# Kernel optimization log

Hardware: AMD Instinct MI355X
Metric: run time of the kernel (lower is better)

The kernel has to match this reference:

```python
import jax, jax.numpy as jnp
import numpy as np

P_ASEM = 0.8
IN_SIZE = 128


def setup_inputs() -> dict:
    key = jax.random.key(0)
    k1, k2, k3, k4 = jax.random.split(key, 4)
    B, N, D = 8, 2048, IN_SIZE
    x = jax.random.normal(k1, (B, N, D), dtype=jnp.float32)
    adj = jax.random.uniform(k2, (B, N, N), dtype=jnp.float32)
    # Linear(2D -> 1): weight [1, 2D], bias [1] (torch convention). Store as vector/scalar.
    bound = 1.0 / np.sqrt(2 * D)
    W = jax.random.uniform(k3, (2 * D,), minval=-bound, maxval=bound, dtype=jnp.float32)
    b = jax.random.uniform(k4, (), minval=-bound, maxval=bound, dtype=jnp.float32)
    return {"x": x, "adj": adj, "W": W, "b": b}


def reference(x, adj, W, b):
    # linear(cat(xi, xj)) == x @ W[:D] (row term) + x @ W[D:] (col term) + b
    # This avoids materializing the [B, N, N, 2D] concat tensor.
    D = x.shape[-1]
    si = jnp.einsum('bnd,d->bn', x, W[:D])  # contribution of xi (varies over axis -2)
    sj = jnp.einsum('bnd,d->bn', x, W[D:])  # contribution of xj (varies over axis -1)
    scores = si[:, :, None] + sj[:, None, :] + b  # [B, N, N]
    return P_ASEM * jax.nn.sigmoid(scores) + (1.0 - P_ASEM) * adj
```

## Files before the change

kernel.cpp:

```cpp
#include <hip/hip_runtime.h>

#define BSZ   8
#define NN    2048
#define DD    128
#define NROWS (BSZ * NN)
#define N4    (NN / 4)
#define P_A   0.8f
#define P_B   0.2f

__global__ __launch_bounds__(256) void row_dots(const float* __restrict__ x,
                                                const float* __restrict__ W,
                                                const float* __restrict__ bias,
                                                float* __restrict__ si,
                                                float* __restrict__ sj) {
    int gtid = blockIdx.x * blockDim.x + threadIdx.x;
    int row  = gtid >> 6;
    int lane = threadIdx.x & 63;
    if (row >= NROWS) return;

    const float* xr = x + (size_t)row * DD;
    float x0 = xr[lane];
    float x1 = xr[lane + 64];

    float a = x0 * W[lane]       + x1 * W[lane + 64];
    float c = x0 * W[lane + 128] + x1 * W[lane + 192];

    #pragma unroll
    for (int off = 32; off > 0; off >>= 1) {
        a += __shfl_down(a, off, 64);
        c += __shfl_down(c, off, 64);
    }
    if (lane == 0) {
        si[row] = a + bias[0];
        sj[row] = c;
    }
}

__global__ __launch_bounds__(256) void fuse_kernel(const float4* __restrict__ adj,
                                                   const float*  __restrict__ si,
                                                   const float4* __restrict__ sj,
                                                   float4* __restrict__ out) {
    int idx = blockIdx.x * blockDim.x + threadIdx.x;
    int j4  = idx & (N4 - 1);
    int row = idx >> 9;
    int b   = row >> 11;

    float  s   = si[row];
    float4 sv  = sj[(b << 9) + j4];
    float4 av  = adj[idx];

    float t0 = s + sv.x;
    float t1 = s + sv.y;
    float t2 = s + sv.z;
    float t3 = s + sv.w;

    float4 o;
    o.x = P_A * (1.0f / (1.0f + __expf(-t0))) + P_B * av.x;
    o.y = P_A * (1.0f / (1.0f + __expf(-t1))) + P_B * av.y;
    o.z = P_A * (1.0f / (1.0f + __expf(-t2))) + P_B * av.z;
    o.w = P_A * (1.0f / (1.0f + __expf(-t3))) + P_B * av.w;

    out[idx] = o;
}

extern "C" void kernel_launch(void* const* d_in, const int* in_sizes, int n_in,
                              void* d_out, int out_size, void* d_ws, size_t ws_size,
                              hipStream_t stream) {
    const float* x    = (const float*)d_in[0];
    const float* adj  = (const float*)d_in[1];
    const float* W    = (const float*)d_in[2];
    const float* bias = (const float*)d_in[3];

    float* si = (float*)d_ws;
    float* sj = si + NROWS;

    row_dots<<<NROWS / 4, 256, 0, stream>>>(x, W, bias, si, sj);

    const int total4 = BSZ * NN * NN / 4;
    fuse_kernel<<<total4 / 256, 256, 0, stream>>>(
        (const float4*)adj, si, (const float4*)sj, (float4*)d_out);
}
```

Before: 236.6 us.

## Process 8 rows per block with nontemporal loads/stores and fast rcp sigmoid

The fuse kernel now gives each block 8 full output rows, and each thread handles two float4 chunks per row. Loads of adj and stores of out use nontemporal hints so the streaming traffic does not pollute the cache. The sigmoid uses the hardware reciprocal intrinsic in place of IEEE division. row_dots computes two rows per wave with float2 loads. This cuts the grid size and per-element overhead at the cost of fewer threads in flight and slightly lower reciprocal precision.

```diff
diff --git a/kernel.cpp b/kernel.cpp
--- a/kernel.cpp
+++ b/kernel.cpp
@@ -8,59 +8,81 @@
 #define P_A   0.8f
 #define P_B   0.2f
 
+typedef float v4f __attribute__((ext_vector_type(4)));
+
 __global__ __launch_bounds__(256) void row_dots(const float* __restrict__ x,
                                                 const float* __restrict__ W,
                                                 const float* __restrict__ bias,
                                                 float* __restrict__ si,
                                                 float* __restrict__ sj) {
     int gtid = blockIdx.x * blockDim.x + threadIdx.x;
-    int row  = gtid >> 6;
+    int wave = gtid >> 6;
     int lane = threadIdx.x & 63;
-    if (row >= NROWS) return;
+    int row0 = wave * 2;
+    if (row0 >= NROWS) return;
 
-    const float* xr = x + (size_t)row * DD;
-    float x0 = xr[lane];
-    float x1 = xr[lane + 64];
+    const float2* xr0 = (const float2*)(x + (size_t)row0 * DD);
+    const float2* xr1 = (const float2*)(x + (size_t)(row0 + 1) * DD);
+    const float2* W2  = (const float2*)W;
 
-    float a = x0 * W[lane]       + x1 * W[lane + 64];
-    float c = x0 * W[lane + 128] + x1 * W[lane + 192];
+    float2 wi = W2[lane];
+    float2 wj = W2[lane + 64];
+    float2 a0 = xr0[lane];
+    float2 a1 = xr1[lane];
+
+    float si0 = a0.x * wi.x + a0.y * wi.y;
+    float sj0 = a0.x * wj.x + a0.y * wj.y;
+    float si1 = a1.x * wi.x + a1.y * wi.y;
+    float sj1 = a1.x * wj.x + a1.y * wj.y;
 
     #pragma unroll
     for (int off = 32; off > 0; off >>= 1) {
-        a += __shfl_down(a, off, 64);
-        c += __shfl_down(c, off, 64);
+        si0 += __shfl_down(si0, off, 64);
+        sj0 += __shfl_down(sj0, off, 64);
+        si1 += __shfl_down(si1, off, 64);
+        sj1 += __shfl_down(sj1, off, 64);
     }
     if (lane == 0) {
-        si[row] = a + bias[0];
-        sj[row] = c;
+        float bb = bias[0];
+        si[row0]     = si0 + bb;
+        si[row0 + 1] = si1 + bb;
+        sj[row0]     = sj0;
+        sj[row0 + 1] = sj1;
     }
 }
 
-__global__ __launch_bounds__(256) void fuse_kernel(const float4* __restrict__ adj,
-                                                   const float*  __restrict__ si,
-                                                   const float4* __restrict__ sj,
-                                                   float4* __restrict__ out) {
-    int idx = blockIdx.x * blockDim.x + threadIdx.x;
-    int j4  = idx & (N4 - 1);
-    int row = idx >> 9;
-    int b   = row >> 11;
+__global__ __launch_bounds__(256) void fuse_kernel(const v4f* __restrict__ adj,
+                                                   const float* __restrict__ si,
+                                                   const v4f* __restrict__ sj,
+                                                   v4f* __restrict__ out) {
+    const int tid = threadIdx.x;
 
-    float  s   = si[row];
-    float4 sv  = sj[(b << 9) + j4];
-    float4 av  = adj[idx];
+    #pragma unroll 2
+    for (int r = 0; r < 8; ++r) {
+        const int row = blockIdx.x * 8 + r;
+        const int b   = row >> 11;
+        const float s = si[row];
+        const v4f* sjrow = sj + (b << 9);
+        const size_t base = (size_t)row * N4;
 
-    float t0 = s + sv.x;
-    float t1 = s + sv.y;
-    float t2 = s + sv.z;
-    float t3 = s + sv.w;
+        v4f sv0 = sjrow[tid];
+        v4f sv1 = sjrow[tid + 256];
+        v4f av0 = __builtin_nontemporal_load(adj + base + tid);
+        v4f av1 = __builtin_nontemporal_load(adj + base + tid + 256);
 
-    float4 o;
-    o.x = P_A * (1.0f / (1.0f + __expf(-t0))) + P_B * av.x;
-    o.y = P_A * (1.0f / (1.0f + __expf(-t1))) + P_B * av.y;
-    o.z = P_A * (1.0f / (1.0f + __expf(-t2))) + P_B * av.z;
-    o.w = P_A * (1.0f / (1.0f + __expf(-t3))) + P_B * av.w;
+        v4f o0, o1;
+        o0.x = P_A * __builtin_amdgcn_rcpf(1.0f + __expf(-(s + sv0.x))) + P_B * av0.x;
+        o0.y = P_A * __builtin_amdgcn_rcpf(1.0f + __expf(-(s + sv0.y))) + P_B * av0.y;
+        o0.z = P_A * __builtin_amdgcn_rcpf(1.0f + __expf(-(s + sv0.z))) + P_B * av0.z;
+        o0.w = P_A * __builtin_amdgcn_rcpf(1.0f + __expf(-(s + sv0.w))) + P_B * av0.w;
+        o1.x = P_A * __builtin_amdgcn_rcpf(1.0f + __expf(-(s + sv1.x))) + P_B * av1.x;
+        o1.y = P_A * __builtin_amdgcn_rcpf(1.0f + __expf(-(s + sv1.y))) + P_B * av1.y;
+        o1.z = P_A * __builtin_amdgcn_rcpf(1.0f + __expf(-(s + sv1.z))) + P_B * av1.z;
+        o1.w = P_A * __builtin_amdgcn_rcpf(1.0f + __expf(-(s + sv1.w))) + P_B * av1.w;
 
-    out[idx] = o;
+        __builtin_nontemporal_store(o0, out + base + tid);
+        __builtin_nontemporal_store(o1, out + base + tid + 256);
+    }
 }
 
 extern "C" void kernel_launch(void* const* d_in, const int* in_sizes, int n_in,
@@ -74,9 +96,8 @@
     float* si = (float*)d_ws;
     float* sj = si + NROWS;
 
-    row_dots<<<NROWS / 4, 256, 0, stream>>>(x, W, bias, si, sj);
+    row_dots<<<NROWS / 8, 256, 0, stream>>>(x, W, bias, si, sj);
 
-    const int total4 = BSZ * NN * NN / 4;
-    fuse_kernel<<<total4 / 256, 256, 0, stream>>>(
-        (const float4*)adj, si, (const float4*)sj, (float4*)d_out);
+    fuse_kernel<<<NROWS / 8, 256, 0, stream>>>(
+        (const v4f*)adj, si, (const v4f*)sj, (v4f*)d_out);
 }
```

Measured after the change: 236.6 us. About the same (-0.0%).
